# Kernel optimization log

Measured on AMD Instinct MI355X. Metric: run time of the kernel, lower is better.

## Reference

```python
import jax, jax.numpy as jnp
import numpy as np
import math

EPS_NORM = 1e-12
BN_EPS = 1e-5


def _l2norm(x):
    n = jnp.sqrt(jnp.sum(x * x, axis=-1, keepdims=True))
    return x / jnp.maximum(n, EPS_NORM)


def setup_inputs() -> dict:
    key = jax.random.key(0)
    ks = jax.random.split(key, 16)
    b, c, t, l = 16, 32, 16, 256
    s = 0.05
    return {
        "x": jax.random.normal(ks[0], (b, c, t, l), jnp.float32),
        "q_w": jax.random.normal(ks[1], (c, c), jnp.float32) * s,
        "q_b": jax.random.normal(ks[2], (c,), jnp.float32) * s,
        "k_w": jax.random.normal(ks[3], (c, c), jnp.float32) * s,
        "k_b": jax.random.normal(ks[4], (c,), jnp.float32) * s,
        "v_w": jax.random.normal(ks[5], (c, c), jnp.float32) * s,
        "v_b": jax.random.normal(ks[6], (c,), jnp.float32) * s,
        "m_w": jax.random.normal(ks[7], (c, c), jnp.float32) * s,
        "m_b": jax.random.normal(ks[8], (c,), jnp.float32) * s,
        "pre_prompt": jax.random.normal(ks[9], (1, c, 1, l), jnp.float32) * s,
        "conv_w": jax.random.normal(ks[10], (c, c, 9, 1), jnp.float32) * s,
        "conv_b": jax.random.normal(ks[11], (c,), jnp.float32) * s,
        "bn_gamma": jnp.ones((c,), jnp.float32),
        "bn_beta": jnp.zeros((c,), jnp.float32),
        "lin_w": jax.random.normal(ks[12], (l, l), jnp.float32) * s,
        "lin_b": jax.random.normal(ks[13], (l,), jnp.float32) * s,
        "atten_flag": 1,
    }


def reference(x, q_w, q_b, k_w, k_b, v_w, v_b, m_w, m_b, pre_prompt,
              conv_w, conv_b, bn_gamma, bn_beta, lin_w, lin_b, atten_flag):
    b, c, t, l = x.shape
    nh = 8
    hd = c // nh

    xp = jnp.transpose(x, (0, 2, 3, 1))  # (b,t,l,c)

    def heads(w, bias):
        h = xp @ w.T + bias
        h = h.reshape(b, t, l, nh, hd).transpose(0, 1, 3, 2, 4)  # (b,t,nh,l,hd)
        return _l2norm(h)

    q = heads(q_w, q_b)
    k = heads(k_w, k_b)
    v = heads(v_w, v_b)

    atten = jnp.einsum('bthld,bthmd->bthlm', q, k) / math.sqrt(hd)
    atten = jax.nn.softmax(atten, axis=-1)
    o = jnp.einsum('bthlm,bthmd->bthld', atten, v)  # (b,t,nh,l,hd)
    o = o.transpose(0, 1, 3, 2, 4).reshape(b, t, l, c)
    o = o @ m_w.T + m_b
    xo = jnp.transpose(o, (0, 3, 1, 2))  # (b,c,t,l)

    pre = jnp.broadcast_to(pre_prompt, (b, c, 1, l))
    con = jnp.concatenate([xo[:, :, :8], pre], axis=2)  # (b,c,9,l)

    # ConvNormAct: Conv2d (VALID, kernel (9,1)) + BatchNorm2d (batch stats) + ReLU
    h = jax.lax.conv_general_dilated(
        con, conv_w, window_strides=(1, 1), padding='VALID',
        dimension_numbers=('NCHW', 'OIHW', 'NCHW'))  # (b,c,1,l)
    h = h + conv_b[None, :, None, None]
    mean = jnp.mean(h, axis=(0, 2, 3), keepdims=True)
    var = jnp.var(h, axis=(0, 2, 3), keepdims=True)
    h = (h - mean) * jax.lax.rsqrt(var + BN_EPS)
    h = h * bn_gamma[None, :, None, None] + bn_beta[None, :, None, None]
    h = jax.nn.relu(h)

    p = h @ lin_w.T + lin_b  # Linear over token_len axis
    p = xo[:, :, 2:3] - p
    return jnp.concatenate([xo[:, :, :8], p], axis=2)  # (b,c,9,l)
```

## Files before the change

### kernel.cpp

```cpp
#include <hip/hip_runtime.h>
#include <hip/hip_bf16.h>


typedef __fp16 h2 __attribute__((ext_vector_type(2)));

#define O_OFF  0u
#define XO_OFF 2097152u
#define H_OFF  6291456u
#define S_OFF  6815744u

__device__ __forceinline__ int probe_f32(const unsigned short* graw) {
    return graw[0] == 0;
}
template<typename T> __device__ __forceinline__ float ldv(const T* p, long i);
template<> __device__ __forceinline__ float ldv<float>(const float* p, long i) {
    return p[i];
}
template<> __device__ __forceinline__ float ldv<__hip_bfloat16>(const __hip_bfloat16* p, long i) {
    return __bfloat162float(p[i]);
}
template<typename T> __device__ __forceinline__ void stv(T* p, size_t i, float v);
template<> __device__ __forceinline__ void stv<float>(float* p, size_t i, float v) {
    p[i] = v;
}
template<> __device__ __forceinline__ void stv<__hip_bfloat16>(__hip_bfloat16* p, size_t i, float v) {
    p[i] = __float2bfloat16(v);
}
__device__ __forceinline__ h2 pkh2(float a, float b) {
    return __builtin_amdgcn_cvt_pkrtz(a, b);
}
union KVrow { uint4 u; h2 h[4]; };

template<typename T>
__device__ __forceinline__ void attn_body(
    const T* __restrict__ x,
    const T* __restrict__ qw, const T* __restrict__ qb,
    const T* __restrict__ kw, const T* __restrict__ kb,
    const T* __restrict__ vw, const T* __restrict__ vb,
    unsigned short* __restrict__ O, uint4* KV)
{
    const int tid = threadIdx.x;
    const int blk = blockIdx.x;
    const int h  = blk & 7;
    const int bt = blk >> 3;
    const int b  = bt >> 3, t = bt & 7;
    const int h4 = h * 4;

    float xv0[32], xv1[32];
    #pragma unroll
    for (int c = 0; c < 32; c++) {
        const long xb = (((long)b * 32 + c) * 16 + t) * 256 + tid;
        xv0[c] = ldv(x, xb);
        xv1[c] = ldv(x, xb + 128);
    }

    float4 pr0[3], pr1[3];
    #pragma unroll
    for (int p = 0; p < 3; p++) {
        const T* W = (p == 0) ? qw : ((p == 1) ? kw : vw);
        const T* B = (p == 0) ? qb : ((p == 1) ? kb : vb);
        float a0[4], a1[4];
        #pragma unroll
        for (int j = 0; j < 4; j++) {
            float bj = ldv(B, h4 + j);
            a0[j] = bj; a1[j] = bj;
        }
        #pragma unroll
        for (int c = 0; c < 32; c++) {
            float x0 = xv0[c], x1 = xv1[c];
            #pragma unroll
            for (int j = 0; j < 4; j++) {
                float w = ldv(W, (long)(h4 + j) * 32 + c);
                a0[j] = fmaf(x0, w, a0[j]);
                a1[j] = fmaf(x1, w, a1[j]);
            }
        }
        float s20 = a0[0]*a0[0] + a0[1]*a0[1] + a0[2]*a0[2] + a0[3]*a0[3];
        float s21 = a1[0]*a1[0] + a1[1]*a1[1] + a1[2]*a1[2] + a1[3]*a1[3];
        float i0 = 1.0f / fmaxf(sqrtf(s20), 1e-12f);
        float i1 = 1.0f / fmaxf(sqrtf(s21), 1e-12f);
        if (p == 0) { i0 *= 0.7213475204444817f; i1 *= 0.7213475204444817f; }
        pr0[p] = make_float4(a0[0]*i0, a0[1]*i0, a0[2]*i0, a0[3]*i0);
        pr1[p] = make_float4(a1[0]*i1, a1[1]*i1, a1[2]*i1, a1[3]*i1);
    }

    KVrow r0, r1;
    r0.h[0] = pkh2(pr0[1].x, pr0[1].y); r0.h[1] = pkh2(pr0[1].z, pr0[1].w);
    r0.h[2] = pkh2(pr0[2].x, pr0[2].y); r0.h[3] = pkh2(pr0[2].z, pr0[2].w);
    r1.h[0] = pkh2(pr1[1].x, pr1[1].y); r1.h[1] = pkh2(pr1[1].z, pr1[1].w);
    r1.h[2] = pkh2(pr1[2].x, pr1[2].y); r1.h[3] = pkh2(pr1[2].z, pr1[2].w);
    KV[tid]       = r0.u;
    KV[tid + 128] = r1.u;
    const float4 qa = pr0[0], qb4 = pr1[0];
    __syncthreads();

    float o0x=0.f,o0y=0.f,o0z=0.f,o0w=0.f,den0=0.f;
    float o1x=0.f,o1y=0.f,o1z=0.f,o1w=0.f,den1=0.f;
    #pragma unroll 8
    for (int m = 0; m < 256; m++) {
        KVrow kv; kv.u = KV[m];
        float k0 = (float)kv.h[0][0], k1 = (float)kv.h[0][1];
        float k2 = (float)kv.h[1][0], k3 = (float)kv.h[1][1];
        float sa = fmaf(qa.x, k0, fmaf(qa.y, k1, fmaf(qa.z, k2, qa.w * k3)));
        float sb = fmaf(qb4.x, k0, fmaf(qb4.y, k1, fmaf(qb4.z, k2, qb4.w * k3)));
        float ea = __builtin_amdgcn_exp2f(sa);
        float eb = __builtin_amdgcn_exp2f(sb);
        float vx = (float)kv.h[2][0], vy = (float)kv.h[2][1];
        float vz = (float)kv.h[3][0], vw = (float)kv.h[3][1];
        den0 += ea; den1 += eb;
        o0x = fmaf(ea, vx, o0x); o0y = fmaf(ea, vy, o0y);
        o0z = fmaf(ea, vz, o0z); o0w = fmaf(ea, vw, o0w);
        o1x = fmaf(eb, vx, o1x); o1y = fmaf(eb, vy, o1y);
        o1z = fmaf(eb, vz, o1z); o1w = fmaf(eb, vw, o1w);
    }
    float i0 = 1.0f / den0, i1 = 1.0f / den1;

    uint2 pk0, pk1;
    h2 a01 = pkh2(o0x*i0, o0y*i0), a23 = pkh2(o0z*i0, o0w*i0);
    h2 b01 = pkh2(o1x*i1, o1y*i1), b23 = pkh2(o1z*i1, o1w*i1);
    pk0.x = *(unsigned int*)&a01; pk0.y = *(unsigned int*)&a23;
    pk1.x = *(unsigned int*)&b01; pk1.y = *(unsigned int*)&b23;
    *(uint2*)(O + ((size_t)bt * 256u + tid) * 32u + h4)       = pk0;
    *(uint2*)(O + ((size_t)bt * 256u + tid + 128) * 32u + h4) = pk1;
}

__global__ __launch_bounds__(128) void k_attn(
    const void* __restrict__ x,
    const void* __restrict__ qw, const void* __restrict__ qb,
    const void* __restrict__ kw, const void* __restrict__ kb,
    const void* __restrict__ vw, const void* __restrict__ vb,
    unsigned short* __restrict__ O, float* __restrict__ sbuf,
    const unsigned short* __restrict__ graw)
{
    __shared__ uint4 KV[256];
    if (blockIdx.x == 0 && threadIdx.x < 64) sbuf[threadIdx.x] = 0.0f;
    if (probe_f32(graw))
        attn_body<float>((const float*)x, (const float*)qw, (const float*)qb,
                         (const float*)kw, (const float*)kb,
                         (const float*)vw, (const float*)vb, O, KV);
    else
        attn_body<__hip_bfloat16>((const __hip_bfloat16*)x,
                                  (const __hip_bfloat16*)qw, (const __hip_bfloat16*)qb,
                                  (const __hip_bfloat16*)kw, (const __hip_bfloat16*)kb,
                                  (const __hip_bfloat16*)vw, (const __hip_bfloat16*)vb, O, KV);
}

template<typename T>
__device__ __forceinline__ void mproj_body(
    const unsigned short* __restrict__ O,
    const T* __restrict__ mw, const T* __restrict__ mb,
    T* __restrict__ out, float* __restrict__ xof)
{
    const int tid = threadIdx.x;
    const int blk = blockIdx.x;
    const int b = blk >> 3, t = blk & 7;

    float ov[32];
    const unsigned short* src = O + ((size_t)blk * 256u + tid) * 32u;
    #pragma unroll
    for (int cc = 0; cc < 4; cc++) {
        union { uint4 u; h2 h[4]; } uu;
        uu.u = *(const uint4*)(src + cc * 8);
        #pragma unroll
        for (int j = 0; j < 4; j++) {
            ov[cc*8 + 2*j]     = (float)uu.h[j][0];
            ov[cc*8 + 2*j + 1] = (float)uu.h[j][1];
        }
    }

    #pragma unroll 4
    for (int co = 0; co < 32; co++) {
        float s = ldv(mb, co);
        #pragma unroll
        for (int c = 0; c < 32; c++)
            s = fmaf(ov[c], ldv(mw, (long)co * 32 + c), s);
        stv(out, (((size_t)b * 32 + co) * 9 + t) * 256u + tid, s);
        xof[(((size_t)b * 32 + co) * 8 + t) * 256u + tid] = s;
    }
}

__global__ __launch_bounds__(256) void k_mproj(
    const unsigned short* __restrict__ O,
    const void* __restrict__ mw, const void* __restrict__ mb,
    void* __restrict__ out, float* __restrict__ xof,
    const unsigned short* __restrict__ graw)
{
    if (probe_f32(graw))
        mproj_body<float>(O, (const float*)mw, (const float*)mb, (float*)out, xof);
    else
        mproj_body<__hip_bfloat16>(O, (const __hip_bfloat16*)mw,
                                   (const __hip_bfloat16*)mb,
                                   (__hip_bfloat16*)out, xof);
}

template<typename T>
__device__ __forceinline__ void conv_body(
    const float* __restrict__ xof, const T* __restrict__ pre,
    const T* __restrict__ cw, const T* __restrict__ cb,
    float* __restrict__ hout, float* __restrict__ s)
{
    const int tid = threadIdx.x;
    const int blk = blockIdx.x;
    const int b = blk >> 3, co0 = (blk & 7) * 4;
    const int l = tid;

    float a0 = 0.f, a1 = 0.f, a2 = 0.f, a3 = 0.f;
    #pragma unroll 2
    for (int ci = 0; ci < 32; ci++) {
        const float* xp = xof + (((size_t)b * 32 + ci) * 8) * 256u + l;
        float v[9];
        #pragma unroll
        for (int kt = 0; kt < 8; kt++) v[kt] = xp[kt * 256];
        v[8] = ldv(pre, (long)ci * 256 + l);
        #pragma unroll
        for (int kt = 0; kt < 9; kt++) {
            const long wb = (long)ci * 9 + kt;
            a0 = fmaf(v[kt], ldv(cw, (long)(co0+0)*288 + wb), a0);
            a1 = fmaf(v[kt], ldv(cw, (long)(co0+1)*288 + wb), a1);
            a2 = fmaf(v[kt], ldv(cw, (long)(co0+2)*288 + wb), a2);
            a3 = fmaf(v[kt], ldv(cw, (long)(co0+3)*288 + wb), a3);
        }
    }
    a0 += ldv(cb, co0+0); a1 += ldv(cb, co0+1);
    a2 += ldv(cb, co0+2); a3 += ldv(cb, co0+3);

    hout[((size_t)b * 32 + co0 + 0) * 256u + l] = a0;
    hout[((size_t)b * 32 + co0 + 1) * 256u + l] = a1;
    hout[((size_t)b * 32 + co0 + 2) * 256u + l] = a2;
    hout[((size_t)b * 32 + co0 + 3) * 256u + l] = a3;

    float acc[4] = {a0, a1, a2, a3};
    #pragma unroll
    for (int g = 0; g < 4; g++) {
        float sg = acc[g], sq = acc[g] * acc[g];
        #pragma unroll
        for (int off = 32; off > 0; off >>= 1) {
            sg += __shfl_down(sg, off, 64);
            sq += __shfl_down(sq, off, 64);
        }
        if ((tid & 63) == 0) {
            atomicAdd(&s[co0 + g], sg);
            atomicAdd(&s[32 + co0 + g], sq);
        }
    }
}

__global__ __launch_bounds__(256) void k_conv(
    const float* __restrict__ xof, const void* __restrict__ pre,
    const void* __restrict__ cw, const void* __restrict__ cb,
    float* __restrict__ hout, float* __restrict__ s,
    const unsigned short* __restrict__ graw)
{
    if (probe_f32(graw))
        conv_body<float>(xof, (const float*)pre, (const float*)cw,
                         (const float*)cb, hout, s);
    else
        conv_body<__hip_bfloat16>(xof, (const __hip_bfloat16*)pre,
                                  (const __hip_bfloat16*)cw,
                                  (const __hip_bfloat16*)cb, hout, s);
}

template<typename T>
__device__ __forceinline__ void lin_body(
    const float* __restrict__ hbuf, const float* __restrict__ s,
    const T* __restrict__ gam, const T* __restrict__ bet,
    const T* __restrict__ lw, const T* __restrict__ lb,
    const float* __restrict__ xof, T* __restrict__ out, float* hn)
{
    const int tid = threadIdx.x;
    const int blk = blockIdx.x;
    const int b = blk >> 5, co = blk & 31;

    float mean = s[co] * (1.0f / 4096.0f);
    float var  = fmaxf(s[32 + co] * (1.0f / 4096.0f) - mean * mean, 0.0f);
    float sc = ldv(gam, co) * __frsqrt_rn(var + 1e-5f);
    float sh = ldv(bet, co) - mean * sc;

    float hv = hbuf[(size_t)blk * 256u + tid];
    hn[tid] = fmaxf(fmaf(hv, sc, sh), 0.0f);
    __syncthreads();

    const T* rp = lw + (size_t)tid * 256u;
    float acc = 0.f;
    #pragma unroll 8
    for (int i = 0; i < 256; i++)
        acc = fmaf(hn[i], ldv(rp, i), acc);
    acc += ldv(lb, tid);

    float xo2 = xof[(((size_t)b * 32 + co) * 8 + 2) * 256u + tid];
    stv(out, (((size_t)b * 32 + co) * 9 + 8) * 256u + tid, xo2 - acc);
}

__global__ __launch_bounds__(256) void k_lin(
    const float* __restrict__ hbuf, const float* __restrict__ s,
    const void* __restrict__ gam, const void* __restrict__ bet,
    const void* __restrict__ lw, const void* __restrict__ lb,
    const float* __restrict__ xof, void* __restrict__ out,
    const unsigned short* __restrict__ graw)
{
    __shared__ float hn[256];
    if (probe_f32(graw))
        lin_body<float>(hbuf, s, (const float*)gam, (const float*)bet,
                        (const float*)lw, (const float*)lb, xof, (float*)out, hn);
    else
        lin_body<__hip_bfloat16>(hbuf, s, (const __hip_bfloat16*)gam,
                                 (const __hip_bfloat16*)bet,
                                 (const __hip_bfloat16*)lw,
                                 (const __hip_bfloat16*)lb, xof,
                                 (__hip_bfloat16*)out, hn);
}

extern "C" void kernel_launch(void* const* d_in, const int* in_sizes, int n_in,
                              void* d_out, int out_size, void* d_ws, size_t ws_size,
                              hipStream_t stream) {
    const unsigned short* graw = (const unsigned short*)d_in[12];

    unsigned short* Obuf = (unsigned short*)((char*)d_ws + O_OFF);
    float* xof  = (float*)((char*)d_ws + XO_OFF);
    float* hbuf = (float*)((char*)d_ws + H_OFF);
    float* sbuf = (float*)((char*)d_ws + S_OFF);

    k_attn <<<1024, 128, 0, stream>>>(d_in[0], d_in[1], d_in[2], d_in[3],
                                      d_in[4], d_in[5], d_in[6],
                                      Obuf, sbuf, graw);
    k_mproj<<<128,  256, 0, stream>>>(Obuf, d_in[7], d_in[8], d_out, xof, graw);
    k_conv <<<128,  256, 0, stream>>>(xof, d_in[9], d_in[10], d_in[11],
                                      hbuf, sbuf, graw);
    k_lin  <<<512,  256, 0, stream>>>(hbuf, sbuf, d_in[12], d_in[13],
                                      d_in[14], d_in[15], xof, d_out, graw);
}
```

Before: 194.6 us.

## Stage weights in LDS and split mproj/conv blocks across token halves

Projection, mproj and conv weights are now staged once per block into shared memory and read back as float4 vectors, replacing repeated scalar global loads inside the FMA loops. The mproj and conv kernels move to 128-thread blocks over token halves, doubling the grid to use more CUs. The linear kernel's row dot product now reads weights as vectorised float4 or packed bf16 loads. Trade-offs are extra syncthreads and LDS staging per block, and more total weight reloads across the larger grids.

```diff
diff --git a/kernel.cpp b/kernel.cpp
--- a/kernel.cpp
+++ b/kernel.cpp
@@ -28,6 +28,12 @@
 }
 __device__ __forceinline__ h2 pkh2(float a, float b) {
     return __builtin_amdgcn_cvt_pkrtz(a, b);
+}
+__device__ __forceinline__ float bflo(unsigned int u) {
+    union { unsigned int i; float f; } c; c.i = u << 16; return c.f;
+}
+__device__ __forceinline__ float bfhi(unsigned int u) {
+    union { unsigned int i; float f; } c; c.i = u & 0xffff0000u; return c.f;
 }
 union KVrow { uint4 u; h2 h[4]; };
 
@@ -37,7 +43,8 @@
     const T* __restrict__ qw, const T* __restrict__ qb,
     const T* __restrict__ kw, const T* __restrict__ kb,
     const T* __restrict__ vw, const T* __restrict__ vb,
-    unsigned short* __restrict__ O, uint4* KV)
+    unsigned short* __restrict__ O, uint4* KV,
+    float (*WL)[4][32], float (*BL)[4])
 {
     const int tid = threadIdx.x;
     const int blk = blockIdx.x;
@@ -46,6 +53,17 @@
     const int b  = bt >> 3, t = bt & 7;
     const int h4 = h * 4;
 
+    for (int e = tid; e < 384; e += 128) {
+        int p = e >> 7, r = e & 127;
+        const T* W = (p == 0) ? qw : ((p == 1) ? kw : vw);
+        WL[p][r >> 5][r & 31] = ldv(W, (long)(h4 + (r >> 5)) * 32 + (r & 31));
+    }
+    if (tid < 12) {
+        int p = tid >> 2, j = tid & 3;
+        const T* B = (p == 0) ? qb : ((p == 1) ? kb : vb);
+        BL[p][j] = ldv(B, h4 + j);
+    }
+
     float xv0[32], xv1[32];
     #pragma unroll
     for (int c = 0; c < 32; c++) {
@@ -53,26 +71,30 @@
         xv0[c] = ldv(x, xb);
         xv1[c] = ldv(x, xb + 128);
     }
+    __syncthreads();
 
     float4 pr0[3], pr1[3];
     #pragma unroll
     for (int p = 0; p < 3; p++) {
-        const T* W = (p == 0) ? qw : ((p == 1) ? kw : vw);
-        const T* B = (p == 0) ? qb : ((p == 1) ? kb : vb);
         float a0[4], a1[4];
         #pragma unroll
-        for (int j = 0; j < 4; j++) {
-            float bj = ldv(B, h4 + j);
-            a0[j] = bj; a1[j] = bj;
-        }
-        #pragma unroll
-        for (int c = 0; c < 32; c++) {
-            float x0 = xv0[c], x1 = xv1[c];
+        for (int j = 0; j < 4; j++) { a0[j] = BL[p][j]; a1[j] = a0[j]; }
+        #pragma unroll
+        for (int c0 = 0; c0 < 32; c0 += 4) {
+            float4 w0 = *(const float4*)&WL[p][0][c0];
+            float4 w1 = *(const float4*)&WL[p][1][c0];
+            float4 w2 = *(const float4*)&WL[p][2][c0];
+            float4 w3 = *(const float4*)&WL[p][3][c0];
+            const float* wj[4] = {(const float*)&w0, (const float*)&w1,
+                                  (const float*)&w2, (const float*)&w3};
             #pragma unroll
-            for (int j = 0; j < 4; j++) {
-                float w = ldv(W, (long)(h4 + j) * 32 + c);
-                a0[j] = fmaf(x0, w, a0[j]);
-                a1[j] = fmaf(x1, w, a1[j]);
+            for (int cc = 0; cc < 4; cc++) {
+                float x0 = xv0[c0+cc], x1 = xv1[c0+cc];
+                #pragma unroll
+                for (int j = 0; j < 4; j++) {
+                    a0[j] = fmaf(x0, wj[j][cc], a0[j]);
+                    a1[j] = fmaf(x1, wj[j][cc], a1[j]);
+                }
             }
         }
         float s20 = a0[0]*a0[0] + a0[1]*a0[1] + a0[2]*a0[2] + a0[3]*a0[3];
@@ -133,30 +155,38 @@
     const unsigned short* __restrict__ graw)
 {
     __shared__ uint4 KV[256];
+    __shared__ float WL[3][4][32];
+    __shared__ float BL[3][4];
     if (blockIdx.x == 0 && threadIdx.x < 64) sbuf[threadIdx.x] = 0.0f;
     if (probe_f32(graw))
         attn_body<float>((const float*)x, (const float*)qw, (const float*)qb,
                          (const float*)kw, (const float*)kb,
-                         (const float*)vw, (const float*)vb, O, KV);
+                         (const float*)vw, (const float*)vb, O, KV, WL, BL);
     else
         attn_body<__hip_bfloat16>((const __hip_bfloat16*)x,
                                   (const __hip_bfloat16*)qw, (const __hip_bfloat16*)qb,
                                   (const __hip_bfloat16*)kw, (const __hip_bfloat16*)kb,
-                                  (const __hip_bfloat16*)vw, (const __hip_bfloat16*)vb, O, KV);
+                                  (const __hip_bfloat16*)vw, (const __hip_bfloat16*)vb,
+                                  O, KV, WL, BL);
 }
 
 template<typename T>
 __device__ __forceinline__ void mproj_body(
     const unsigned short* __restrict__ O,
     const T* __restrict__ mw, const T* __restrict__ mb,
-    T* __restrict__ out, float* __restrict__ xof)
+    T* __restrict__ out, float* __restrict__ xof, float* sw, float* sb)
 {
     const int tid = threadIdx.x;
     const int blk = blockIdx.x;
-    const int b = blk >> 3, t = blk & 7;
+    const int bt = blk >> 1, lhalf = blk & 1;
+    const int b = bt >> 3, t = bt & 7;
+    const int l = lhalf * 128 + tid;
+
+    for (int e = tid; e < 1024; e += 128) sw[e] = ldv(mw, e);
+    if (tid < 32) sb[tid] = ldv(mb, tid);
 
     float ov[32];
-    const unsigned short* src = O + ((size_t)blk * 256u + tid) * 32u;
+    const unsigned short* src = O + ((size_t)bt * 256u + l) * 32u;
     #pragma unroll
     for (int cc = 0; cc < 4; cc++) {
         union { uint4 u; h2 h[4]; } uu;
@@ -167,45 +197,61 @@
             ov[cc*8 + 2*j + 1] = (float)uu.h[j][1];
         }
     }
+    __syncthreads();
 
     #pragma unroll 4
     for (int co = 0; co < 32; co++) {
-        float s = ldv(mb, co);
-        #pragma unroll
-        for (int c = 0; c < 32; c++)
-            s = fmaf(ov[c], ldv(mw, (long)co * 32 + c), s);
-        stv(out, (((size_t)b * 32 + co) * 9 + t) * 256u + tid, s);
-        xof[(((size_t)b * 32 + co) * 8 + t) * 256u + tid] = s;
-    }
-}
-
-__global__ __launch_bounds__(256) void k_mproj(
+        float s = sb[co];
+        #pragma unroll
+        for (int c0 = 0; c0 < 32; c0 += 4) {
+            float4 w4 = *(const float4*)&sw[co * 32 + c0];
+            s = fmaf(ov[c0+0], w4.x, s);
+            s = fmaf(ov[c0+1], w4.y, s);
+            s = fmaf(ov[c0+2], w4.z, s);
+            s = fmaf(ov[c0+3], w4.w, s);
+        }
+        stv(out, (((size_t)b * 32 + co) * 9 + t) * 256u + l, s);
+        xof[(((size_t)b * 32 + co) * 8 + t) * 256u + l] = s;
+    }
+}
+
+__global__ __launch_bounds__(128) void k_mproj(
     const unsigned short* __restrict__ O,
     const void* __restrict__ mw, const void* __restrict__ mb,
     void* __restrict__ out, float* __restrict__ xof,
     const unsigned short* __restrict__ graw)
 {
+    __shared__ float sw[1024];
+    __shared__ float sb[32];
     if (probe_f32(graw))
-        mproj_body<float>(O, (const float*)mw, (const float*)mb, (float*)out, xof);
+        mproj_body<float>(O, (const float*)mw, (const float*)mb,
+                          (float*)out, xof, sw, sb);
     else
         mproj_body<__hip_bfloat16>(O, (const __hip_bfloat16*)mw,
                                    (const __hip_bfloat16*)mb,
-                                   (__hip_bfloat16*)out, xof);
+                                   (__hip_bfloat16*)out, xof, sw, sb);
 }
 
 template<typename T>
 __device__ __forceinline__ void conv_body(
     const float* __restrict__ xof, const T* __restrict__ pre,
     const T* __restrict__ cw, const T* __restrict__ cb,
-    float* __restrict__ hout, float* __restrict__ s)
+    float* __restrict__ hout, float* __restrict__ s, float* wl)
 {
     const int tid = threadIdx.x;
     const int blk = blockIdx.x;
-    const int b = blk >> 3, co0 = (blk & 7) * 4;
-    const int l = tid;
+    const int b = blk >> 4, cog = (blk >> 1) & 7, lhalf = blk & 1;
+    const int co0 = cog * 4;
+    const int l = lhalf * 128 + tid;
+
+    for (int e = tid; e < 1152; e += 128) {
+        int g = e & 3, r = e >> 2;
+        wl[e] = ldv(cw, (long)(co0 + g) * 288 + r);
+    }
+    __syncthreads();
 
     float a0 = 0.f, a1 = 0.f, a2 = 0.f, a3 = 0.f;
-    #pragma unroll 2
+    #pragma unroll 4
     for (int ci = 0; ci < 32; ci++) {
         const float* xp = xof + (((size_t)b * 32 + ci) * 8) * 256u + l;
         float v[9];
@@ -214,11 +260,11 @@
         v[8] = ldv(pre, (long)ci * 256 + l);
         #pragma unroll
         for (int kt = 0; kt < 9; kt++) {
-            const long wb = (long)ci * 9 + kt;
-            a0 = fmaf(v[kt], ldv(cw, (long)(co0+0)*288 + wb), a0);
-            a1 = fmaf(v[kt], ldv(cw, (long)(co0+1)*288 + wb), a1);
-            a2 = fmaf(v[kt], ldv(cw, (long)(co0+2)*288 + wb), a2);
-            a3 = fmaf(v[kt], ldv(cw, (long)(co0+3)*288 + wb), a3);
+            float4 w4 = *(const float4*)&wl[(ci * 9 + kt) * 4];
+            a0 = fmaf(v[kt], w4.x, a0);
+            a1 = fmaf(v[kt], w4.y, a1);
+            a2 = fmaf(v[kt], w4.z, a2);
+            a3 = fmaf(v[kt], w4.w, a3);
         }
     }
     a0 += ldv(cb, co0+0); a1 += ldv(cb, co0+1);
@@ -245,19 +291,49 @@
     }
 }
 
-__global__ __launch_bounds__(256) void k_conv(
+__global__ __launch_bounds__(128) void k_conv(
     const float* __restrict__ xof, const void* __restrict__ pre,
     const void* __restrict__ cw, const void* __restrict__ cb,
     float* __restrict__ hout, float* __restrict__ s,
     const unsigned short* __restrict__ graw)
 {
+    __shared__ float wl[1152];
     if (probe_f32(graw))
         conv_body<float>(xof, (const float*)pre, (const float*)cw,
-                         (const float*)cb, hout, s);
+                         (const float*)cb, hout, s, wl);
     else
         conv_body<__hip_bfloat16>(xof, (const __hip_bfloat16*)pre,
                                   (const __hip_bfloat16*)cw,
-                                  (const __hip_bfloat16*)cb, hout, s);
+                                  (const __hip_bfloat16*)cb, hout, s, wl);
+}
+
+__device__ __forceinline__ float rowdot(const float* rp, const float* hn) {
+    float acc = 0.f;
+    #pragma unroll 4
+    for (int i0 = 0; i0 < 256; i0 += 4) {
+        float4 u = *(const float4*)(rp + i0);
+        acc = fmaf(hn[i0+0], u.x, acc);
+        acc = fmaf(hn[i0+1], u.y, acc);
+        acc = fmaf(hn[i0+2], u.z, acc);
+        acc = fmaf(hn[i0+3], u.w, acc);
+    }
+    return acc;
+}
+__device__ __forceinline__ float rowdot(const __hip_bfloat16* rp_, const float* hn) {
+    const unsigned short* rp = (const unsigned short*)rp_;
+    float acc = 0.f;
+    #pragma unroll 2
+    for (int i0 = 0; i0 < 256; i0 += 16) {
+        uint4 u0 = *(const uint4*)(rp + i0);
+        uint4 u1 = *(const uint4*)(rp + i0 + 8);
+        unsigned int uu[8] = {u0.x, u0.y, u0.z, u0.w, u1.x, u1.y, u1.z, u1.w};
+        #pragma unroll
+        for (int j = 0; j < 8; j++) {
+            acc = fmaf(hn[i0 + 2*j],     bflo(uu[j]), acc);
+            acc = fmaf(hn[i0 + 2*j + 1], bfhi(uu[j]), acc);
+        }
+    }
+    return acc;
 }
 
 template<typename T>
@@ -280,12 +356,7 @@
     hn[tid] = fmaxf(fmaf(hv, sc, sh), 0.0f);
     __syncthreads();
 
-    const T* rp = lw + (size_t)tid * 256u;
-    float acc = 0.f;
-    #pragma unroll 8
-    for (int i = 0; i < 256; i++)
-        acc = fmaf(hn[i], ldv(rp, i), acc);
-    acc += ldv(lb, tid);
+    float acc = rowdot(lw + (size_t)tid * 256u, hn) + ldv(lb, tid);
 
     float xo2 = xof[(((size_t)b * 32 + co) * 8 + 2) * 256u + tid];
     stv(out, (((size_t)b * 32 + co) * 9 + 8) * 256u + tid, xo2 - acc);
@@ -323,8 +394,8 @@
     k_attn <<<1024, 128, 0, stream>>>(d_in[0], d_in[1], d_in[2], d_in[3],
                                       d_in[4], d_in[5], d_in[6],
                                       Obuf, sbuf, graw);
-    k_mproj<<<128,  256, 0, stream>>>(Obuf, d_in[7], d_in[8], d_out, xof, graw);
-    k_conv <<<128,  256, 0, stream>>>(xof, d_in[9], d_in[10], d_in[11],
+    k_mproj<<<256,  128, 0, stream>>>(Obuf, d_in[7], d_in[8], d_out, xof, graw);
+    k_conv <<<256,  128, 0, stream>>>(xof, d_in[9], d_in[10], d_in[11],
                                       hbuf, sbuf, graw);
     k_lin  <<<512,  256, 0, stream>>>(hbuf, sbuf, d_in[12], d_in[13],
                                       d_in[14], d_in[15], xof, d_out, graw);
```

Measured after the change: 190.1 us. -2.3%, faster.
